# Optimization experiments

Hardware: AMD Instinct MI355X
Metric: run time of the kernel (lower is better)

Reference implementation:

```python
import jax, jax.numpy as jnp
import numpy as np

N = 50000
NEG_SLOPE = 0.2  # PyG GATConv default negative_slope


def _gat_layer(x, src, dst, edge_attr, W, We, a_src, a_dst, a_edge, bias):
    """Single-head PyG GATConv (heads=1, concat=True, add_self_loops=True,
    fill_value='mean' for self-loop edge_attr, dropout inactive / eval mode)."""
    n = x.shape[0]
    # add self loops; self-loop edge_attr = per-feature mean of edge_attr
    loop = jnp.arange(n)
    src2 = jnp.concatenate([src, loop])
    dst2 = jnp.concatenate([dst, loop])
    ea_loop = jnp.broadcast_to(edge_attr.mean(axis=0, keepdims=True), (n, edge_attr.shape[1]))
    ea = jnp.concatenate([edge_attr, ea_loop], axis=0)          # [E', edge_dim]

    h = x @ W                                                    # [N, C_out]
    a_s = h @ a_src                                              # [N]
    a_d = h @ a_dst                                              # [N]
    a_e = (ea @ We) @ a_edge                                     # [E']

    alpha = jax.nn.leaky_relu(a_s[src2] + a_d[dst2] + a_e, NEG_SLOPE)  # [E']
    # segment softmax over incoming edges of each dst node
    amax = jax.ops.segment_max(alpha, dst2, num_segments=n)     # [N]
    ex = jnp.exp(alpha - amax[dst2])                             # [E']
    denom = jax.ops.segment_sum(ex, dst2, num_segments=n)       # [N]
    w = ex / denom[dst2]                                         # [E']

    msg = h[src2] * w[:, None]                                   # [E', C_out]
    out = jax.ops.segment_sum(msg, dst2, num_segments=n) + bias  # [N, C_out]
    return out


def setup_inputs() -> dict:
    key = jax.random.key(0)
    ks = jax.random.split(key, 16)
    E, C_in, C_h, C_out, Ed = 800000, 128, 256, 128, 8
    s = 0.05
    inp = {
        "x": jax.random.normal(ks[0], (N, C_in), dtype=jnp.float32),
        "edge_index": jax.random.randint(ks[1], (2, E), 0, N, dtype=jnp.int32),
        "edge_attr": jax.random.normal(ks[2], (E, Ed), dtype=jnp.float32),
        # layer 1 params
        "W1": jax.random.normal(ks[3], (C_in, C_h), dtype=jnp.float32) * s,
        "We1": jax.random.normal(ks[4], (Ed, C_h), dtype=jnp.float32) * s,
        "as1": jax.random.normal(ks[5], (C_h,), dtype=jnp.float32) * s,
        "ad1": jax.random.normal(ks[6], (C_h,), dtype=jnp.float32) * s,
        "ae1": jax.random.normal(ks[7], (C_h,), dtype=jnp.float32) * s,
        "b1": jnp.zeros((C_h,), dtype=jnp.float32),
        # layer 2 params
        "W2": jax.random.normal(ks[8], (C_h, C_out), dtype=jnp.float32) * s,
        "We2": jax.random.normal(ks[9], (Ed, C_out), dtype=jnp.float32) * s,
        "as2": jax.random.normal(ks[10], (C_out,), dtype=jnp.float32) * s,
        "ad2": jax.random.normal(ks[11], (C_out,), dtype=jnp.float32) * s,
        "ae2": jax.random.normal(ks[12], (C_out,), dtype=jnp.float32) * s,
        "b2": jnp.zeros((C_out,), dtype=jnp.float32),
    }
    return inp


def reference(x, edge_index, edge_attr, W1, We1, as1, ad1, ae1, b1,
              W2, We2, as2, ad2, ae2, b2):
    src, dst = edge_index[0], edge_index[1]
    h = _gat_layer(x, src, dst, edge_attr, W1, We1, as1, ad1, ae1, b1)
    h = jax.nn.relu(h)  # relu between layers, not after last
    out = _gat_layer(h, src, dst, edge_attr, W2, We2, as2, ad2, ae2, b2)
    return out
```

## Files before the change

### kernel.cpp

```cpp
#include <hip/hip_runtime.h>
#include <hip/hip_bf16.h>


#define NEG_SLOPE 0.2f

typedef unsigned short u16;
typedef short short8 __attribute__((ext_vector_type(8)));
typedef float v4f __attribute__((ext_vector_type(4)));
typedef u16 u16x8 __attribute__((ext_vector_type(8)));

__device__ __forceinline__ u16 f2bf(float f) {
    unsigned u = __float_as_uint(f);
    return (u16)((u + 0x7fffu + ((u >> 16) & 1u)) >> 16);
}
__device__ __forceinline__ float bf2f(u16 h) {
    return __uint_as_float(((unsigned)h) << 16);
}
__device__ __forceinline__ float bf_lo(int v) { return __uint_as_float(((unsigned)v) << 16); }
__device__ __forceinline__ float bf_hi(int v) { return __uint_as_float(((unsigned)v) & 0xffff0000u); }
__device__ __forceinline__ float lrelu(float x) {
    return x >= 0.f ? x : NEG_SLOPE * x;
}
__device__ __forceinline__ int ld_acq(int* p) {
    return __hip_atomic_load(p, __ATOMIC_ACQUIRE, __HIP_MEMORY_SCOPE_AGENT);
}
__device__ __forceinline__ void st_rel(int* p, int v) {
    __hip_atomic_store(p, v, __ATOMIC_RELEASE, __HIP_MEMORY_SCOPE_AGENT);
}

__global__ __launch_bounds__(256) void prep_kernel(
        const float* __restrict__ W1, u16* __restrict__ w1thi, u16* __restrict__ w1tlo,
        const float* __restrict__ W2, u16* __restrict__ w2thi, u16* __restrict__ w2tlo,
        const float* __restrict__ We1, const float* __restrict__ ae1v,
        const float* __restrict__ We2, const float* __restrict__ ae2v,
        float* __restrict__ we_vec1g, float* __restrict__ we_vec2g) {
    int tid = threadIdx.x;
    if (blockIdx.x < 256) {
        int t = blockIdx.x * 256 + tid;
        if (t < 128 * 256) {
            int k = t >> 8, m = t & 255;
            float v = W1[t];
            u16 h = f2bf(v);
            w1thi[(size_t)m * 128 + k] = h;
            w1tlo[(size_t)m * 128 + k] = f2bf(v - bf2f(h));
        } else {
            t -= 128 * 256;
            int k = t >> 7, m = t & 127;
            float v = W2[t];
            u16 h = f2bf(v);
            w2thi[(size_t)m * 256 + k] = h;
            w2tlo[(size_t)m * 256 + k] = f2bf(v - bf2f(h));
        }
        return;
    }
    __shared__ float wv[16];
    if (tid < 16) wv[tid] = 0.f;
    __syncthreads();
    {
        float a1 = ae1v[tid];
        int lane = tid & 63;
#pragma unroll
        for (int j = 0; j < 8; ++j) {
            float v = We1[j * 256 + tid] * a1;
#pragma unroll
            for (int o = 32; o; o >>= 1) v += __shfl_down(v, o);
            if (lane == 0) atomicAdd(&wv[j], v);
        }
        if (tid < 128) {
            float a2 = ae2v[tid];
#pragma unroll
            for (int j = 0; j < 8; ++j) {
                float v = We2[j * 128 + tid] * a2;
#pragma unroll
                for (int o = 32; o; o >>= 1) v += __shfl_down(v, o);
                if (lane == 0) atomicAdd(&wv[8 + j], v);
            }
        }
    }
    __syncthreads();
    if (tid < 8)  we_vec1g[tid] = wv[tid];
    else if (tid < 16) we_vec2g[tid - 8] = wv[tid];
}

#define BK 32
#define LDA 40
__global__ __launch_bounds__(256) void fat1_kernel(
        const float* __restrict__ ea, const int* __restrict__ dst,
        float* __restrict__ mean_acc, int* __restrict__ deg,
        int* __restrict__ rank, float2* __restrict__ aEe, int E,
        const float* __restrict__ we_vec1g, const float* __restrict__ we_vec2g,
        int Fb, int Gg,
        const float* __restrict__ A32,
        const u16* __restrict__ Bh_g, const u16* __restrict__ Bl_g,
        u16* __restrict__ Cb, int Nrows, int K, int M,
        const float* __restrict__ av, const float* __restrict__ bv,
        float* __restrict__ as_out, float* __restrict__ ad_out, int gx) {
    __shared__ u16 Ah[64 * LDA];
    __shared__ u16 Bh[128 * LDA];
    __shared__ u16 Bl[128 * LDA];
    __shared__ float red[8];
    int tid = threadIdx.x;
    int bid = (int)blockIdx.x;
    int mn = Fb < Gg ? Fb : Gg;
    int hid = -1, gid = -1;
    if (bid < 2 * mn) {
        if ((bid & 1) == 0) hid = bid >> 1; else gid = bid >> 1;
    } else {
        int rem = bid - 2 * mn;
        if (Fb > Gg) hid = mn + rem; else gid = mn + rem;
    }
    if (hid >= 0) {
        float wv[16];
#pragma unroll
        for (int j = 0; j < 8; ++j) { wv[j] = we_vec1g[j]; wv[8 + j] = we_vec2g[j]; }
        if (tid < 8) red[tid] = 0.f;
        __syncthreads();
        float s[8] = {0.f};
        int stride = Fb * 256;
        for (int e = hid * 256 + tid; e < E; e += stride) {
            int d = dst[e];
            const float4 v0 = *(const float4*)&ea[(size_t)e * 8];
            const float4 v1 = *(const float4*)&ea[(size_t)e * 8 + 4];
            s[0] += v0.x; s[1] += v0.y; s[2] += v0.z; s[3] += v0.w;
            s[4] += v1.x; s[5] += v1.y; s[6] += v1.z; s[7] += v1.w;
            float s1 = v0.x * wv[0] + v0.y * wv[1] + v0.z * wv[2] + v0.w * wv[3]
                     + v1.x * wv[4] + v1.y * wv[5] + v1.z * wv[6] + v1.w * wv[7];
            float s2 = v0.x * wv[8] + v0.y * wv[9] + v0.z * wv[10] + v0.w * wv[11]
                     + v1.x * wv[12] + v1.y * wv[13] + v1.z * wv[14] + v1.w * wv[15];
            aEe[e] = make_float2(s1, s2);
            rank[e] = atomicAdd(&deg[d], 1);
        }
        int lane = tid & 63;
#pragma unroll
        for (int j = 0; j < 8; ++j) {
#pragma unroll
            for (int o = 32; o; o >>= 1) s[j] += __shfl_down(s[j], o);
            if (lane == 0) atomicAdd(&red[j], s[j]);
        }
        __syncthreads();
        if (tid < 8) atomicAdd(&mean_acc[tid], red[tid]);
        return;
    }
    int lane = tid & 63;
    int wvx = tid >> 6;
    int l15 = lane & 15, quad = lane >> 4;
    int rb = (gid / gx) * 64;
    int cb = (gid % gx) * 128;

    v4f acc[8];
#pragma unroll
    for (int ni = 0; ni < 8; ++ni) acc[ni] = (v4f){0.f, 0.f, 0.f, 0.f};

    int sr  = tid >> 2;
    int sc  = (tid & 3) * 8;
    int sr2 = tid >> 1;
    int sc2 = (tid & 1) * 16;

    for (int kc = 0; kc < K; kc += BK) {
        int gr = rb + sr;
        u16x8 a0 = {0,0,0,0,0,0,0,0};
        if (gr < Nrows) {
            const float* pa = A32 + (size_t)gr * K + kc + sc;
            float4 f0 = *(const float4*)pa;
            float4 f1 = *(const float4*)(pa + 4);
            a0 = (u16x8){f2bf(f0.x), f2bf(f0.y), f2bf(f0.z), f2bf(f0.w),
                         f2bf(f1.x), f2bf(f1.y), f2bf(f1.z), f2bf(f1.w)};
        }
        size_t bb = (size_t)(cb + sr2) * K + kc + sc2;
        u16x8 b0 = *(const u16x8*)(Bh_g + bb);
        u16x8 b1 = *(const u16x8*)(Bh_g + bb + 8);
        u16x8 b2 = *(const u16x8*)(Bl_g + bb);
        u16x8 b3 = *(const u16x8*)(Bl_g + bb + 8);
        *(u16x8*)&Ah[sr * LDA + sc] = a0;
        *(u16x8*)&Bh[sr2 * LDA + sc2] = b0;
        *(u16x8*)&Bh[sr2 * LDA + sc2 + 8] = b1;
        *(u16x8*)&Bl[sr2 * LDA + sc2] = b2;
        *(u16x8*)&Bl[sr2 * LDA + sc2 + 8] = b3;
        __syncthreads();
        short8 ah = *(const short8*)&Ah[(wvx * 16 + l15) * LDA + quad * 8];
#pragma unroll
        for (int ni = 0; ni < 8; ++ni) {
            int r = (ni * 16 + l15) * LDA + quad * 8;
            short8 bhf = *(const short8*)&Bh[r];
            short8 blf = *(const short8*)&Bl[r];
            acc[ni] = __builtin_amdgcn_mfma_f32_16x16x32_bf16(ah, bhf, acc[ni], 0, 0, 0);
            acc[ni] = __builtin_amdgcn_mfma_f32_16x16x32_bf16(ah, blf, acc[ni], 0, 0, 0);
        }
        __syncthreads();
    }
#pragma unroll
    for (int ni = 0; ni < 8; ++ni)
#pragma unroll
        for (int reg = 0; reg < 4; ++reg) {
            int row = rb + wvx * 16 + quad * 4 + reg;
            if (row < Nrows)
                Cb[(size_t)row * M + cb + ni * 16 + l15] = f2bf(acc[ni][reg]);
        }
    float sd[4] = {}, dd[4] = {};
#pragma unroll
    for (int ni = 0; ni < 8; ++ni) {
        int col = cb + ni * 16 + l15;
        float a = av[col], b = bv[col];
#pragma unroll
        for (int reg = 0; reg < 4; ++reg) {
            sd[reg] += acc[ni][reg] * a;
            dd[reg] += acc[ni][reg] * b;
        }
    }
#pragma unroll
    for (int off = 1; off < 16; off <<= 1)
#pragma unroll
        for (int reg = 0; reg < 4; ++reg) {
            sd[reg] += __shfl_xor(sd[reg], off);
            dd[reg] += __shfl_xor(dd[reg], off);
        }
    if (l15 == 0) {
        int row0 = rb + wvx * 16 + quad * 4;
#pragma unroll
        for (int reg = 0; reg < 4; ++reg)
            if (row0 + reg < Nrows) {
                atomicAdd(as_out + row0 + reg, sd[reg]);
                atomicAdd(ad_out + row0 + reg, dd[reg]);
            }
    }
}

__global__ __launch_bounds__(256) void scan_fused_kernel(
        const int* __restrict__ deg, int* __restrict__ row_start,
        int* __restrict__ partials, int* __restrict__ pprefix,
        int* __restrict__ gcount, int* __restrict__ gflag, int N, int n,
        const float* __restrict__ mean_acc, float Einv,
        const float* __restrict__ we_vec1, const float* __restrict__ we_vec2,
        float* __restrict__ ae_loop) {
    __shared__ int s[256];
    __shared__ int amLast, bprefix;
    int t = threadIdx.x, bid = blockIdx.x;
    int i = bid * 256 + t;
    int v = (i < N) ? deg[i] : 0;
    s[t] = v; __syncthreads();
    for (int off = 1; off < 256; off <<= 1) {
        int u = (t >= off) ? s[t - off] : 0;
        __syncthreads();
        s[t] += u;
        __syncthreads();
    }
    int incl = s[t];
    int total = s[255];
    if (t == 0) {
        partials[bid] = total;
        __threadfence();
        int c = __hip_atomic_fetch_add(gcount, 1, __ATOMIC_ACQ_REL, __HIP_MEMORY_SCOPE_AGENT);
        amLast = (c == (int)gridDim.x - 1);
    }
    __syncthreads();
    if (amLast) {
        int G = gridDim.x;
        int pv = (t < G) ? ld_acq(&partials[t]) : 0;
        __syncthreads();
        s[t] = pv; __syncthreads();
        for (int off = 1; off < 256; off <<= 1) {
            int u = (t >= off) ? s[t - off] : 0;
            __syncthreads();
            s[t] += u;
            __syncthreads();
        }
        if (t < G) pprefix[t] = s[t] - pv;
        if (t == 0) {
            float s1 = 0.f, s2 = 0.f;
#pragma unroll
            for (int j = 0; j < 8; ++j) {
                float m = mean_acc[j] * Einv;
                s1 += m * we_vec1[j];
                s2 += m * we_vec2[j];
            }
            ae_loop[0] = s1; ae_loop[1] = s2;
        }
        __threadfence();
        __syncthreads();
        if (t == 0) st_rel(gflag, 1);
    }
    if (t == 0) {
        while (ld_acq(gflag) == 0) __builtin_amdgcn_s_sleep(2);
        bprefix = ld_acq(&pprefix[bid]);
    }
    __syncthreads();
    int ex = bprefix + incl - v;
    if (i < n) row_start[i] = ex;
}

__global__ __launch_bounds__(256) void fill_kernel(
        const int* __restrict__ src, const int* __restrict__ dst,
        const float2* __restrict__ aEe, const int* __restrict__ row_start,
        const int* __restrict__ rank,
        const float* __restrict__ asv1, const float* __restrict__ adv1,
        float4* __restrict__ epack, int E) {
    int e = blockIdx.x * 256 + threadIdx.x;
    if (e >= E) return;
    int d = dst[e];
    int s = src[e];
    int idx = row_start[d] + rank[e];
    float2 a = aEe[e];
    float w = __expf(lrelu(asv1[s] + adv1[d] + a.x));
    epack[idx] = make_float4(__int_as_float(s), w, a.y, 0.f);
}

#define LDA2 40
__global__ __launch_bounds__(256) void gemm_mfma_kernel(
        const u16* __restrict__ A_g,
        const u16* __restrict__ Bh_g, const u16* __restrict__ Bl_g,
        u16* __restrict__ Cb, int Nrows, int K, int M,
        const float* __restrict__ av, const float* __restrict__ bv,
        float* __restrict__ as_out, float* __restrict__ ad_out) {
    __shared__ u16 Ah[128 * LDA2], Bh[128 * LDA2], Bl[128 * LDA2];
    int tid = threadIdx.x;
    int lane = tid & 63;
    int wv = tid >> 6;
    int wm = wv >> 1, wn = wv & 1;
    int l15 = lane & 15, quad = lane >> 4;
    int rb = blockIdx.y * 128;
    int cb = blockIdx.x * 128;

    v4f acc[4][4];
#pragma unroll
    for (int mi = 0; mi < 4; ++mi)
#pragma unroll
        for (int ni = 0; ni < 4; ++ni) acc[mi][ni] = (v4f){0.f, 0.f, 0.f, 0.f};

    int sr = tid >> 1;
    int sc = (tid & 1) * 16;

    for (int kc = 0; kc < K; kc += BK) {
        int gr = rb + sr;
        u16x8 a0 = {0,0,0,0,0,0,0,0}, a1 = {0,0,0,0,0,0,0,0};
        if (gr < Nrows) {
            size_t ba = (size_t)gr * K + kc + sc;
            a0 = *(const u16x8*)(A_g + ba);
            a1 = *(const u16x8*)(A_g + ba + 8);
        }
        size_t bb = (size_t)(cb + sr) * K + kc + sc;
        u16x8 b0 = *(const u16x8*)(Bh_g + bb);
        u16x8 b1 = *(const u16x8*)(Bh_g + bb + 8);
        u16x8 b2 = *(const u16x8*)(Bl_g + bb);
        u16x8 b3 = *(const u16x8*)(Bl_g + bb + 8);
        *(u16x8*)&Ah[sr * LDA2 + sc] = a0;
        *(u16x8*)&Ah[sr * LDA2 + sc + 8] = a1;
        *(u16x8*)&Bh[sr * LDA2 + sc] = b0;
        *(u16x8*)&Bh[sr * LDA2 + sc + 8] = b1;
        *(u16x8*)&Bl[sr * LDA2 + sc] = b2;
        *(u16x8*)&Bl[sr * LDA2 + sc + 8] = b3;
        __syncthreads();
        short8 ah[4], bh[4], bl[4];
#pragma unroll
        for (int mi = 0; mi < 4; ++mi)
            ah[mi] = *(const short8*)&Ah[(wm * 64 + mi * 16 + l15) * LDA2 + quad * 8];
#pragma unroll
        for (int ni = 0; ni < 4; ++ni) {
            int r = (wn * 64 + ni * 16 + l15) * LDA2 + quad * 8;
            bh[ni] = *(const short8*)&Bh[r];
            bl[ni] = *(const short8*)&Bl[r];
        }
#pragma unroll
        for (int mi = 0; mi < 4; ++mi)
#pragma unroll
            for (int ni = 0; ni < 4; ++ni) {
                acc[mi][ni] = __builtin_amdgcn_mfma_f32_16x16x32_bf16(ah[mi], bh[ni], acc[mi][ni], 0, 0, 0);
                acc[mi][ni] = __builtin_amdgcn_mfma_f32_16x16x32_bf16(ah[mi], bl[ni], acc[mi][ni], 0, 0, 0);
            }
        __syncthreads();
    }
#pragma unroll
    for (int mi = 0; mi < 4; ++mi)
#pragma unroll
        for (int ni = 0; ni < 4; ++ni)
#pragma unroll
            for (int reg = 0; reg < 4; ++reg) {
                int row = rb + wm * 64 + mi * 16 + quad * 4 + reg;
                if (row < Nrows)
                    Cb[(size_t)row * M + cb + wn * 64 + ni * 16 + l15] = f2bf(acc[mi][ni][reg]);
            }
    float sd[4][4] = {}, dd[4][4] = {};
#pragma unroll
    for (int ni = 0; ni < 4; ++ni) {
        int col = cb + wn * 64 + ni * 16 + l15;
        float a = av[col], b = bv[col];
#pragma unroll
        for (int mi = 0; mi < 4; ++mi)
#pragma unroll
            for (int reg = 0; reg < 4; ++reg) {
                sd[mi][reg] += acc[mi][ni][reg] * a;
                dd[mi][reg] += acc[mi][ni][reg] * b;
            }
    }
#pragma unroll
    for (int off = 1; off < 16; off <<= 1)
#pragma unroll
        for (int mi = 0; mi < 4; ++mi)
#pragma unroll
            for (int reg = 0; reg < 4; ++reg) {
                sd[mi][reg] += __shfl_xor(sd[mi][reg], off);
                dd[mi][reg] += __shfl_xor(dd[mi][reg], off);
            }
    if (l15 == 0)
#pragma unroll
        for (int mi = 0; mi < 4; ++mi) {
            int row0 = rb + wm * 64 + mi * 16 + quad * 4;
#pragma unroll
            for (int reg = 0; reg < 4; ++reg)
                if (row0 + reg < Nrows) {
                    atomicAdd(as_out + row0 + reg, sd[mi][reg]);
                    atomicAdd(ad_out + row0 + reg, dd[mi][reg]);
                }
        }
}

__global__ __launch_bounds__(256) void agg1_kernel(const int* __restrict__ row_start,
                                                   const float4* __restrict__ epack,
                                                   const float* __restrict__ asv,
                                                   const float* __restrict__ adv,
                                                   const float* __restrict__ ae_loop,
                                                   const u16* __restrict__ Hb,
                                                   u16* __restrict__ ohi,
                                                   const float* __restrict__ bias, int N) {
    __shared__ float2 xch[4][64];
    int lane = threadIdx.x & 63;
    int wvi = threadIdx.x >> 6;
    int node = blockIdx.x * 4 + wvi;
    if (node >= N) return;
    int st = row_start[node], en = row_start[node + 1];
    float wloop = __expf(lrelu(asv[node] + adv[node] + ae_loop[0]));
    float sum = wloop;
    int half = lane >> 5;
    int hl   = lane & 31;
    float acc[8];
    {
        int4 hv = *(const int4*)(Hb + (size_t)node * 256 + hl * 8);
        float w0 = half ? 0.f : wloop;
        acc[0] = w0 * bf_lo(hv.x); acc[1] = w0 * bf_hi(hv.x);
        acc[2] = w0 * bf_lo(hv.y); acc[3] = w0 * bf_hi(hv.y);
        acc[4] = w0 * bf_lo(hv.z); acc[5] = w0 * bf_hi(hv.z);
        acc[6] = w0 * bf_lo(hv.w); acc[7] = w0 * bf_hi(hv.w);
    }
    for (int base = st; base < en; base += 64) {
        int i = base + lane;
        float w = 0.f; int sreg = 0;
        if (i < en) {
            float4 ep = epack[i];
            sreg = __float_as_int(ep.x);
            w = ep.y;
        }
        float wsum = w;
#pragma unroll
        for (int o = 1; o < 64; o <<= 1) wsum += __shfl_xor(wsum, o);
        sum += wsum;
        xch[wvi][lane] = make_float2(w, __int_as_float(sreg));
        int cnt = min(64, en - base);
        int j = 0;
        for (; j + 8 <= cnt; j += 8) {
            float2 e[4]; int4 h[4];
#pragma unroll
            for (int q = 0; q < 4; ++q) e[q] = xch[wvi][j + 2 * q + half];
#pragma unroll
            for (int q = 0; q < 4; ++q)
                h[q] = *(const int4*)(Hb + (size_t)__float_as_int(e[q].y) * 256 + hl * 8);
#pragma unroll
            for (int q = 0; q < 4; ++q) {
                float w0 = e[q].x;
                acc[0] += w0 * bf_lo(h[q].x); acc[1] += w0 * bf_hi(h[q].x);
                acc[2] += w0 * bf_lo(h[q].y); acc[3] += w0 * bf_hi(h[q].y);
                acc[4] += w0 * bf_lo(h[q].z); acc[5] += w0 * bf_hi(h[q].z);
                acc[6] += w0 * bf_lo(h[q].w); acc[7] += w0 * bf_hi(h[q].w);
            }
        }
        for (; j + 2 <= cnt; j += 2) {
            float2 e0 = xch[wvi][j + half];
            int4 h0 = *(const int4*)(Hb + (size_t)__float_as_int(e0.y) * 256 + hl * 8);
            float w0 = e0.x;
            acc[0] += w0 * bf_lo(h0.x); acc[1] += w0 * bf_hi(h0.x);
            acc[2] += w0 * bf_lo(h0.y); acc[3] += w0 * bf_hi(h0.y);
            acc[4] += w0 * bf_lo(h0.z); acc[5] += w0 * bf_hi(h0.z);
            acc[6] += w0 * bf_lo(h0.w); acc[7] += w0 * bf_hi(h0.w);
        }
        if (j < cnt && half == 0) {
            float2 e0 = xch[wvi][j];
            int4 h0 = *(const int4*)(Hb + (size_t)__float_as_int(e0.y) * 256 + hl * 8);
            float w0 = e0.x;
            acc[0] += w0 * bf_lo(h0.x); acc[1] += w0 * bf_hi(h0.x);
            acc[2] += w0 * bf_lo(h0.y); acc[3] += w0 * bf_hi(h0.y);
            acc[4] += w0 * bf_lo(h0.z); acc[5] += w0 * bf_hi(h0.z);
            acc[6] += w0 * bf_lo(h0.w); acc[7] += w0 * bf_hi(h0.w);
        }
    }
#pragma unroll
    for (int c = 0; c < 8; ++c) acc[c] += __shfl_xor(acc[c], 32);
    if (half == 0) {
        float inv = 1.f / sum;
        const float4 b0 = *(const float4*)(bias + hl * 8);
        const float4 b1 = *(const float4*)(bias + hl * 8 + 4);
        float t0 = acc[0] * inv + b0.x, t1 = acc[1] * inv + b0.y;
        float t2 = acc[2] * inv + b0.z, t3 = acc[3] * inv + b0.w;
        float t4 = acc[4] * inv + b1.x, t5 = acc[5] * inv + b1.y;
        float t6 = acc[6] * inv + b1.z, t7 = acc[7] * inv + b1.w;
        t0 = t0 > 0.f ? t0 : 0.f; t1 = t1 > 0.f ? t1 : 0.f;
        t2 = t2 > 0.f ? t2 : 0.f; t3 = t3 > 0.f ? t3 : 0.f;
        t4 = t4 > 0.f ? t4 : 0.f; t5 = t5 > 0.f ? t5 : 0.f;
        t6 = t6 > 0.f ? t6 : 0.f; t7 = t7 > 0.f ? t7 : 0.f;
        u16x8 h;
        h[0] = f2bf(t0); h[1] = f2bf(t1); h[2] = f2bf(t2); h[3] = f2bf(t3);
        h[4] = f2bf(t4); h[5] = f2bf(t5); h[6] = f2bf(t6); h[7] = f2bf(t7);
        *(u16x8*)(ohi + (size_t)node * 256 + hl * 8) = h;
    }
}

__global__ __launch_bounds__(256) void agg2_kernel(const int* __restrict__ row_start,
                                                   const float4* __restrict__ epack,
                                                   const float* __restrict__ asv,
                                                   const float* __restrict__ adv,
                                                   const float* __restrict__ ae_loop,
                                                   const u16* __restrict__ Hb,
                                                   float* __restrict__ out,
                                                   const float* __restrict__ bias, int N) {
    __shared__ float2 xch[4][64];
    int lane = threadIdx.x & 63;
    int wvi = threadIdx.x >> 6;
    int node = blockIdx.x * 4 + wvi;
    if (node >= N) return;
    int st = row_start[node], en = row_start[node + 1];
    float ad = adv[node];
    float wloop = __expf(lrelu(asv[node] + ad + ae_loop[1]));
    float sum = wloop;
    int half = lane >> 5;
    int hl   = lane & 31;
    float acc[4];
    {
        int2 hv = *(const int2*)(Hb + (size_t)node * 128 + hl * 4);
        float w0 = half ? 0.f : wloop;
        acc[0] = w0 * bf_lo(hv.x); acc[1] = w0 * bf_hi(hv.x);
        acc[2] = w0 * bf_lo(hv.y); acc[3] = w0 * bf_hi(hv.y);
    }
    for (int base = st; base < en; base += 64) {
        int i = base + lane;
        float w = 0.f; int sreg = 0;
        if (i < en) {
            float4 ep = epack[i];
            sreg = __float_as_int(ep.x);
            w = __expf(lrelu(asv[sreg] + ad + ep.z));
        }
        float wsum = w;
#pragma unroll
        for (int o = 1; o < 64; o <<= 1) wsum += __shfl_xor(wsum, o);
        sum += wsum;
        xch[wvi][lane] = make_float2(w, __int_as_float(sreg));
        int cnt = min(64, en - base);
        int j = 0;
        for (; j + 8 <= cnt; j += 8) {
            float2 e[4]; int2 h[4];
#pragma unroll
            for (int q = 0; q < 4; ++q) e[q] = xch[wvi][j + 2 * q + half];
#pragma unroll
            for (int q = 0; q < 4; ++q)
                h[q] = *(const int2*)(Hb + (size_t)__float_as_int(e[q].y) * 128 + hl * 4);
#pragma unroll
            for (int q = 0; q < 4; ++q) {
                float w0 = e[q].x;
                acc[0] += w0 * bf_lo(h[q].x); acc[1] += w0 * bf_hi(h[q].x);
                acc[2] += w0 * bf_lo(h[q].y); acc[3] += w0 * bf_hi(h[q].y);
            }
        }
        for (; j + 2 <= cnt; j += 2) {
            float2 e0 = xch[wvi][j + half];
            int2 h0 = *(const int2*)(Hb + (size_t)__float_as_int(e0.y) * 128 + hl * 4);
            float w0 = e0.x;
            acc[0] += w0 * bf_lo(h0.x); acc[1] += w0 * bf_hi(h0.x);
            acc[2] += w0 * bf_lo(h0.y); acc[3] += w0 * bf_hi(h0.y);
        }
        if (j < cnt && half == 0) {
            float2 e0 = xch[wvi][j];
            int2 h0 = *(const int2*)(Hb + (size_t)__float_as_int(e0.y) * 128 + hl * 4);
            float w0 = e0.x;
            acc[0] += w0 * bf_lo(h0.x); acc[1] += w0 * bf_hi(h0.x);
            acc[2] += w0 * bf_lo(h0.y); acc[3] += w0 * bf_hi(h0.y);
        }
    }
#pragma unroll
    for (int c = 0; c < 4; ++c) acc[c] += __shfl_xor(acc[c], 32);
    if (half == 0) {
        float inv = 1.f / sum;
        const float4 bv = *(const float4*)(bias + hl * 4);
        float4 o;
        o.x = acc[0] * inv + bv.x;
        o.y = acc[1] * inv + bv.y;
        o.z = acc[2] * inv + bv.z;
        o.w = acc[3] * inv + bv.w;
        *(float4*)(out + (size_t)node * 128 + hl * 4) = o;
    }
}

extern "C" void kernel_launch(void* const* d_in, const int* in_sizes, int n_in,
                              void* d_out, int out_size, void* d_ws, size_t ws_size,
                              hipStream_t stream) {
    const int Cin = 128, Ch = 256, Co = 128;
    const int N = in_sizes[0] / Cin;
    const int E = in_sizes[1] / 2;

    const float* x   = (const float*)d_in[0];
    const int*   src = (const int*)d_in[1];
    const int*   dst = src + E;
    const float* ea  = (const float*)d_in[2];
    const float* W1  = (const float*)d_in[3];
    const float* We1 = (const float*)d_in[4];
    const float* as1 = (const float*)d_in[5];
    const float* ad1 = (const float*)d_in[6];
    const float* ae1 = (const float*)d_in[7];
    const float* b1  = (const float*)d_in[8];
    const float* W2  = (const float*)d_in[9];
    const float* We2 = (const float*)d_in[10];
    const float* as2 = (const float*)d_in[11];
    const float* ad2 = (const float*)d_in[12];
    const float* ae2 = (const float*)d_in[13];
    const float* b2  = (const float*)d_in[14];
    float* out = (float*)d_out;

    float* ws = (float*)d_ws;
    size_t off = 0;
    u16* h1b = (u16*)(ws + off); off += (size_t)N * Ch / 2;
    u16* g1b = (u16*)(ws + off); off += (size_t)N * Ch / 2;
    float4* epack = (float4*)(ws + off); off += (size_t)E * 4;
    float2* aEe   = (float2*)(ws + off); off += (size_t)E * 2;
    int* rank     = (int*)(ws + off); off += (size_t)E;
    int* row_start = (int*)(ws + off); off += (size_t)N + 1;
    int* partials  = (int*)(ws + off); off += 256;
    int* pprefix   = (int*)(ws + off); off += 256;
    u16* w1thi = (u16*)(ws + off); off += (size_t)Cin * Ch / 2;
    u16* w1tlo = (u16*)(ws + off); off += (size_t)Cin * Ch / 2;
    u16* w2thi = (u16*)(ws + off); off += (size_t)Ch * Co / 2;
    u16* w2tlo = (u16*)(ws + off); off += (size_t)Ch * Co / 2;
    int*   deg  = (int*)(ws + off); off += (size_t)N + 1;
    float* asv1 = ws + off; off += (size_t)N;
    float* adv1 = ws + off; off += (size_t)N;
    float* asv2 = ws + off; off += (size_t)N;
    float* adv2 = ws + off; off += (size_t)N;
    float* misc = ws + off; off += 32;
    float* mean_acc = misc;
    float* we_vec1  = misc + 8;
    float* we_vec2  = misc + 16;
    float* ae_loop  = misc + 24;
    int* gcount = (int*)(ws + off); off += 1;
    int* gflag  = (int*)(ws + off); off += 1;

    const int n1 = N + 1;
    const int nscan = (n1 + 255) / 256;

    hipMemsetAsync(deg, 0, ((size_t)5 * N + 35) * sizeof(float), stream);

    prep_kernel<<<257, 256, 0, stream>>>(
        W1, w1thi, w1tlo, W2, w2thi, w2tlo,
        We1, ae1, We2, ae2, we_vec1, we_vec2);

    {
        int Fb = 1024;
        int gx = Ch / 128;
        int Gg = gx * ((N + 63) / 64);
        fat1_kernel<<<Fb + Gg, 256, 0, stream>>>(
            ea, dst, mean_acc, deg, rank, aEe, E, we_vec1, we_vec2, Fb, Gg,
            x, w1thi, w1tlo, h1b, N, Cin, Ch, as1, ad1, asv1, adv1, gx);
    }

    scan_fused_kernel<<<nscan, 256, 0, stream>>>(
        deg, row_start, partials, pprefix, gcount, gflag, N, n1,
        mean_acc, 1.0f / (float)E, we_vec1, we_vec2, ae_loop);

    fill_kernel<<<(E + 255) / 256, 256, 0, stream>>>(src, dst, aEe, row_start,
                                                     rank, asv1, adv1, epack, E);

    agg1_kernel<<<(N + 3) / 4, 256, 0, stream>>>(row_start, epack, asv1, adv1, ae_loop,
                                                 h1b, g1b, b1, N);

    u16* h2b = h1b;
    {
        dim3 grid(Co / 128, (N + 127) / 128);
        gemm_mfma_kernel<<<grid, 256, 0, stream>>>(g1b, w2thi, w2tlo, h2b, N, Ch, Co,
                                                   as2, ad2, asv2, adv2);
    }
    agg2_kernel<<<(N + 3) / 4, 256, 0, stream>>>(row_start, epack, asv2, adv2, ae_loop,
                                                 h2b, out, b2, N);
}
```

Baseline: 343.6 us.

## Overlap layer-2 GEMM with agg1 tail and precompute layer-2 attention logits

Folds W2·as2 and W2·ad2 into 256-wide vectors so agg1 computes layer-2 source and destination scores directly from its bf16 output, dropping the atomic reductions in the GEMM epilogue. Splits agg1 at a node boundary and launches fused kernels that run the agg1 tail interleaved with GEMM tiles on finished rows, then the remaining GEMM tiles alongside a per-edge pass that precomputes layer-2 edge weights into epack. agg2 then reads the stored weight instead of recomputing the exp. This adds a separate h2b buffer and relies on kernel ordering for correctness, and the split point is hardcoded.

After: 369.9 us. 1.08x slower.

```diff
diff --git a/kernel.cpp b/kernel.cpp
--- a/kernel.cpp
+++ b/kernel.cpp
@@ -33,7 +33,9 @@
         const float* __restrict__ W2, u16* __restrict__ w2thi, u16* __restrict__ w2tlo,
         const float* __restrict__ We1, const float* __restrict__ ae1v,
         const float* __restrict__ We2, const float* __restrict__ ae2v,
-        float* __restrict__ we_vec1g, float* __restrict__ we_vec2g) {
+        float* __restrict__ we_vec1g, float* __restrict__ we_vec2g,
+        const float* __restrict__ as2v, const float* __restrict__ ad2v,
+        float* __restrict__ wa2g, float* __restrict__ wb2g) {
     int tid = threadIdx.x;
     if (blockIdx.x < 256) {
         int t = blockIdx.x * 256 + tid;
@@ -51,6 +53,20 @@
             w2thi[(size_t)m * 256 + k] = h;
             w2tlo[(size_t)m * 256 + k] = f2bf(v - bf2f(h));
         }
+        return;
+    }
+    if (blockIdx.x == 257) {
+        const float* w2row = W2 + (size_t)tid * 128;
+        float da = 0.f, db = 0.f;
+#pragma unroll 8
+        for (int m = 0; m < 128; m += 4) {
+            float4 w = *(const float4*)(w2row + m);
+            float4 a = *(const float4*)(as2v + m);
+            float4 b = *(const float4*)(ad2v + m);
+            da += w.x * a.x + w.y * a.y + w.z * a.z + w.w * a.w;
+            db += w.x * b.x + w.y * b.y + w.z * b.z + w.w * b.w;
+        }
+        wa2g[tid] = da; wb2g[tid] = db;
         return;
     }
     __shared__ float wv[16];
@@ -304,128 +320,15 @@
     epack[idx] = make_float4(__int_as_float(s), w, a.y, 0.f);
 }
 
-#define LDA2 40
-__global__ __launch_bounds__(256) void gemm_mfma_kernel(
-        const u16* __restrict__ A_g,
-        const u16* __restrict__ Bh_g, const u16* __restrict__ Bl_g,
-        u16* __restrict__ Cb, int Nrows, int K, int M,
-        const float* __restrict__ av, const float* __restrict__ bv,
-        float* __restrict__ as_out, float* __restrict__ ad_out) {
-    __shared__ u16 Ah[128 * LDA2], Bh[128 * LDA2], Bl[128 * LDA2];
-    int tid = threadIdx.x;
-    int lane = tid & 63;
-    int wv = tid >> 6;
-    int wm = wv >> 1, wn = wv & 1;
-    int l15 = lane & 15, quad = lane >> 4;
-    int rb = blockIdx.y * 128;
-    int cb = blockIdx.x * 128;
-
-    v4f acc[4][4];
-#pragma unroll
-    for (int mi = 0; mi < 4; ++mi)
-#pragma unroll
-        for (int ni = 0; ni < 4; ++ni) acc[mi][ni] = (v4f){0.f, 0.f, 0.f, 0.f};
-
-    int sr = tid >> 1;
-    int sc = (tid & 1) * 16;
-
-    for (int kc = 0; kc < K; kc += BK) {
-        int gr = rb + sr;
-        u16x8 a0 = {0,0,0,0,0,0,0,0}, a1 = {0,0,0,0,0,0,0,0};
-        if (gr < Nrows) {
-            size_t ba = (size_t)gr * K + kc + sc;
-            a0 = *(const u16x8*)(A_g + ba);
-            a1 = *(const u16x8*)(A_g + ba + 8);
-        }
-        size_t bb = (size_t)(cb + sr) * K + kc + sc;
-        u16x8 b0 = *(const u16x8*)(Bh_g + bb);
-        u16x8 b1 = *(const u16x8*)(Bh_g + bb + 8);
-        u16x8 b2 = *(const u16x8*)(Bl_g + bb);
-        u16x8 b3 = *(const u16x8*)(Bl_g + bb + 8);
-        *(u16x8*)&Ah[sr * LDA2 + sc] = a0;
-        *(u16x8*)&Ah[sr * LDA2 + sc + 8] = a1;
-        *(u16x8*)&Bh[sr * LDA2 + sc] = b0;
-        *(u16x8*)&Bh[sr * LDA2 + sc + 8] = b1;
-        *(u16x8*)&Bl[sr * LDA2 + sc] = b2;
-        *(u16x8*)&Bl[sr * LDA2 + sc + 8] = b3;
-        __syncthreads();
-        short8 ah[4], bh[4], bl[4];
-#pragma unroll
-        for (int mi = 0; mi < 4; ++mi)
-            ah[mi] = *(const short8*)&Ah[(wm * 64 + mi * 16 + l15) * LDA2 + quad * 8];
-#pragma unroll
-        for (int ni = 0; ni < 4; ++ni) {
-            int r = (wn * 64 + ni * 16 + l15) * LDA2 + quad * 8;
-            bh[ni] = *(const short8*)&Bh[r];
-            bl[ni] = *(const short8*)&Bl[r];
-        }
-#pragma unroll
-        for (int mi = 0; mi < 4; ++mi)
-#pragma unroll
-            for (int ni = 0; ni < 4; ++ni) {
-                acc[mi][ni] = __builtin_amdgcn_mfma_f32_16x16x32_bf16(ah[mi], bh[ni], acc[mi][ni], 0, 0, 0);
-                acc[mi][ni] = __builtin_amdgcn_mfma_f32_16x16x32_bf16(ah[mi], bl[ni], acc[mi][ni], 0, 0, 0);
-            }
-        __syncthreads();
-    }
-#pragma unroll
-    for (int mi = 0; mi < 4; ++mi)
-#pragma unroll
-        for (int ni = 0; ni < 4; ++ni)
-#pragma unroll
-            for (int reg = 0; reg < 4; ++reg) {
-                int row = rb + wm * 64 + mi * 16 + quad * 4 + reg;
-                if (row < Nrows)
-                    Cb[(size_t)row * M + cb + wn * 64 + ni * 16 + l15] = f2bf(acc[mi][ni][reg]);
-            }
-    float sd[4][4] = {}, dd[4][4] = {};
-#pragma unroll
-    for (int ni = 0; ni < 4; ++ni) {
-        int col = cb + wn * 64 + ni * 16 + l15;
-        float a = av[col], b = bv[col];
-#pragma unroll
-        for (int mi = 0; mi < 4; ++mi)
-#pragma unroll
-            for (int reg = 0; reg < 4; ++reg) {
-                sd[mi][reg] += acc[mi][ni][reg] * a;
-                dd[mi][reg] += acc[mi][ni][reg] * b;
-            }
-    }
-#pragma unroll
-    for (int off = 1; off < 16; off <<= 1)
-#pragma unroll
-        for (int mi = 0; mi < 4; ++mi)
-#pragma unroll
-            for (int reg = 0; reg < 4; ++reg) {
-                sd[mi][reg] += __shfl_xor(sd[mi][reg], off);
-                dd[mi][reg] += __shfl_xor(dd[mi][reg], off);
-            }
-    if (l15 == 0)
-#pragma unroll
-        for (int mi = 0; mi < 4; ++mi) {
-            int row0 = rb + wm * 64 + mi * 16 + quad * 4;
-#pragma unroll
-            for (int reg = 0; reg < 4; ++reg)
-                if (row0 + reg < Nrows) {
-                    atomicAdd(as_out + row0 + reg, sd[mi][reg]);
-                    atomicAdd(ad_out + row0 + reg, dd[mi][reg]);
-                }
-        }
-}
-
-__global__ __launch_bounds__(256) void agg1_kernel(const int* __restrict__ row_start,
-                                                   const float4* __restrict__ epack,
-                                                   const float* __restrict__ asv,
-                                                   const float* __restrict__ adv,
-                                                   const float* __restrict__ ae_loop,
-                                                   const u16* __restrict__ Hb,
-                                                   u16* __restrict__ ohi,
-                                                   const float* __restrict__ bias, int N) {
-    __shared__ float2 xch[4][64];
-    int lane = threadIdx.x & 63;
-    int wvi = threadIdx.x >> 6;
-    int node = blockIdx.x * 4 + wvi;
-    if (node >= N) return;
+__device__ __forceinline__ void agg1_node(
+        int node, int lane, float2* xw,
+        const int* __restrict__ row_start, const float4* __restrict__ epack,
+        const float* __restrict__ asv, const float* __restrict__ adv,
+        const float* __restrict__ ae_loop,
+        const u16* __restrict__ Hb, u16* __restrict__ ohi,
+        const float* __restrict__ bias,
+        const float* __restrict__ wa2, const float* __restrict__ wb2,
+        float* __restrict__ asv2, float* __restrict__ adv2) {
     int st = row_start[node], en = row_start[node + 1];
     float wloop = __expf(lrelu(asv[node] + adv[node] + ae_loop[0]));
     float sum = wloop;
@@ -452,27 +355,27 @@
 #pragma unroll
         for (int o = 1; o < 64; o <<= 1) wsum += __shfl_xor(wsum, o);
         sum += wsum;
-        xch[wvi][lane] = make_float2(w, __int_as_float(sreg));
-        int cnt = min(64, en - base);
+        xw[lane] = make_float2(w, __int_as_float(sreg));
+        int cnt = en - base; if (cnt > 64) cnt = 64;
         int j = 0;
         for (; j + 8 <= cnt; j += 8) {
-            float2 e[4]; int4 h[4];
-#pragma unroll
-            for (int q = 0; q < 4; ++q) e[q] = xch[wvi][j + 2 * q + half];
+            float2 e[4]; int4 h4[4];
+#pragma unroll
+            for (int q = 0; q < 4; ++q) e[q] = xw[j + 2 * q + half];
 #pragma unroll
             for (int q = 0; q < 4; ++q)
-                h[q] = *(const int4*)(Hb + (size_t)__float_as_int(e[q].y) * 256 + hl * 8);
+                h4[q] = *(const int4*)(Hb + (size_t)__float_as_int(e[q].y) * 256 + hl * 8);
 #pragma unroll
             for (int q = 0; q < 4; ++q) {
                 float w0 = e[q].x;
-                acc[0] += w0 * bf_lo(h[q].x); acc[1] += w0 * bf_hi(h[q].x);
-                acc[2] += w0 * bf_lo(h[q].y); acc[3] += w0 * bf_hi(h[q].y);
-                acc[4] += w0 * bf_lo(h[q].z); acc[5] += w0 * bf_hi(h[q].z);
-                acc[6] += w0 * bf_lo(h[q].w); acc[7] += w0 * bf_hi(h[q].w);
+                acc[0] += w0 * bf_lo(h4[q].x); acc[1] += w0 * bf_hi(h4[q].x);
+                acc[2] += w0 * bf_lo(h4[q].y); acc[3] += w0 * bf_hi(h4[q].y);
+                acc[4] += w0 * bf_lo(h4[q].z); acc[5] += w0 * bf_hi(h4[q].z);
+                acc[6] += w0 * bf_lo(h4[q].w); acc[7] += w0 * bf_hi(h4[q].w);
             }
         }
         for (; j + 2 <= cnt; j += 2) {
-            float2 e0 = xch[wvi][j + half];
+            float2 e0 = xw[j + half];
             int4 h0 = *(const int4*)(Hb + (size_t)__float_as_int(e0.y) * 256 + hl * 8);
             float w0 = e0.x;
             acc[0] += w0 * bf_lo(h0.x); acc[1] += w0 * bf_hi(h0.x);
@@ -481,7 +384,7 @@
             acc[6] += w0 * bf_lo(h0.w); acc[7] += w0 * bf_hi(h0.w);
         }
         if (j < cnt && half == 0) {
-            float2 e0 = xch[wvi][j];
+            float2 e0 = xw[j];
             int4 h0 = *(const int4*)(Hb + (size_t)__float_as_int(e0.y) * 256 + hl * 8);
             float w0 = e0.x;
             acc[0] += w0 * bf_lo(h0.x); acc[1] += w0 * bf_hi(h0.x);
@@ -504,11 +407,152 @@
         t2 = t2 > 0.f ? t2 : 0.f; t3 = t3 > 0.f ? t3 : 0.f;
         t4 = t4 > 0.f ? t4 : 0.f; t5 = t5 > 0.f ? t5 : 0.f;
         t6 = t6 > 0.f ? t6 : 0.f; t7 = t7 > 0.f ? t7 : 0.f;
-        u16x8 h;
-        h[0] = f2bf(t0); h[1] = f2bf(t1); h[2] = f2bf(t2); h[3] = f2bf(t3);
-        h[4] = f2bf(t4); h[5] = f2bf(t5); h[6] = f2bf(t6); h[7] = f2bf(t7);
-        *(u16x8*)(ohi + (size_t)node * 256 + hl * 8) = h;
-    }
+        u16x8 hv8;
+        hv8[0] = f2bf(t0); hv8[1] = f2bf(t1); hv8[2] = f2bf(t2); hv8[3] = f2bf(t3);
+        hv8[4] = f2bf(t4); hv8[5] = f2bf(t5); hv8[6] = f2bf(t6); hv8[7] = f2bf(t7);
+        *(u16x8*)(ohi + (size_t)node * 256 + hl * 8) = hv8;
+        const float* wa = wa2 + hl * 8;
+        const float* wb = wb2 + hl * 8;
+        float da = 0.f, db = 0.f;
+#pragma unroll
+        for (int c = 0; c < 8; ++c) {
+            float r = bf2f(hv8[c]);
+            da += r * wa[c]; db += r * wb[c];
+        }
+#pragma unroll
+        for (int o = 1; o < 32; o <<= 1) {
+            da += __shfl_xor(da, o);
+            db += __shfl_xor(db, o);
+        }
+        if (hl == 0) { asv2[node] = da; adv2[node] = db; }
+    }
+}
+
+__global__ __launch_bounds__(256) void agg1_kernel(
+        int n0, int ncap,
+        const int* __restrict__ row_start, const float4* __restrict__ epack,
+        const float* __restrict__ asv, const float* __restrict__ adv,
+        const float* __restrict__ ae_loop,
+        const u16* __restrict__ Hb, u16* __restrict__ ohi,
+        const float* __restrict__ bias,
+        const float* __restrict__ wa2, const float* __restrict__ wb2,
+        float* __restrict__ asv2, float* __restrict__ adv2) {
+    __shared__ float2 xch[4][64];
+    int lane = threadIdx.x & 63;
+    int wvi = threadIdx.x >> 6;
+    int node = n0 + blockIdx.x * 4 + wvi;
+    if (node >= ncap) return;
+    agg1_node(node, lane, xch[wvi], row_start, epack, asv, adv, ae_loop,
+              Hb, ohi, bias, wa2, wb2, asv2, adv2);
+}
+
+__device__ __forceinline__ void gemm2_tile(
+        int gid, int r0, int Nrows, int tid,
+        const u16* __restrict__ A_g, const u16* __restrict__ Bh_g,
+        const u16* __restrict__ Bl_g, u16* __restrict__ Cb,
+        u16* Ah, u16* Bh, u16* Bl) {
+    const int K = 256, M = 128;
+    int lane = tid & 63;
+    int wvx = tid >> 6;
+    int l15 = lane & 15, quad = lane >> 4;
+    int rb = r0 + gid * 64;
+    v4f acc[8];
+#pragma unroll
+    for (int ni = 0; ni < 8; ++ni) acc[ni] = (v4f){0.f, 0.f, 0.f, 0.f};
+    int sr  = tid >> 2;
+    int sc  = (tid & 3) * 8;
+    int sr2 = tid >> 1;
+    int sc2 = (tid & 1) * 16;
+    for (int kc = 0; kc < K; kc += BK) {
+        int gr = rb + sr;
+        u16x8 a0 = {0,0,0,0,0,0,0,0};
+        if (gr < Nrows) a0 = *(const u16x8*)(A_g + (size_t)gr * K + kc + sc);
+        size_t bb = (size_t)sr2 * K + kc + sc2;
+        u16x8 b0 = *(const u16x8*)(Bh_g + bb);
+        u16x8 b1 = *(const u16x8*)(Bh_g + bb + 8);
+        u16x8 b2 = *(const u16x8*)(Bl_g + bb);
+        u16x8 b3 = *(const u16x8*)(Bl_g + bb + 8);
+        *(u16x8*)&Ah[sr * LDA + sc] = a0;
+        *(u16x8*)&Bh[sr2 * LDA + sc2] = b0;
+        *(u16x8*)&Bh[sr2 * LDA + sc2 + 8] = b1;
+        *(u16x8*)&Bl[sr2 * LDA + sc2] = b2;
+        *(u16x8*)&Bl[sr2 * LDA + sc2 + 8] = b3;
+        __syncthreads();
+        short8 ah = *(const short8*)&Ah[(wvx * 16 + l15) * LDA + quad * 8];
+#pragma unroll
+        for (int ni = 0; ni < 8; ++ni) {
+            int r = (ni * 16 + l15) * LDA + quad * 8;
+            short8 bhf = *(const short8*)&Bh[r];
+            short8 blf = *(const short8*)&Bl[r];
+            acc[ni] = __builtin_amdgcn_mfma_f32_16x16x32_bf16(ah, bhf, acc[ni], 0, 0, 0);
+            acc[ni] = __builtin_amdgcn_mfma_f32_16x16x32_bf16(ah, blf, acc[ni], 0, 0, 0);
+        }
+        __syncthreads();
+    }
+#pragma unroll
+    for (int ni = 0; ni < 8; ++ni)
+#pragma unroll
+        for (int reg = 0; reg < 4; ++reg) {
+            int row = rb + wvx * 16 + quad * 4 + reg;
+            if (row < Nrows)
+                Cb[(size_t)row * M + ni * 16 + l15] = f2bf(acc[ni][reg]);
+        }
+}
+
+__global__ __launch_bounds__(256) void fat23_kernel(
+        int Ga, int n0a, int Ncap,
+        int Gg, int r0g, int NrowsG,
+        int Ge,
+        const int* __restrict__ row_start, const float4* __restrict__ epack,
+        const float* __restrict__ asv1v, const float* __restrict__ adv1v,
+        const float* __restrict__ ae_loop,
+        const u16* __restrict__ h1b, u16* __restrict__ g1b,
+        const float* __restrict__ b1,
+        const float* __restrict__ wa2, const float* __restrict__ wb2,
+        float* __restrict__ asv2, float* __restrict__ adv2,
+        const u16* __restrict__ Ag, const u16* __restrict__ Bh_g,
+        const u16* __restrict__ Bl_g, u16* __restrict__ Cb,
+        const int* __restrict__ src, const int* __restrict__ dst,
+        const int* __restrict__ rank, const float2* __restrict__ aEe,
+        float4* __restrict__ epackw, int E) {
+    __shared__ u16 Ah[64 * LDA];
+    __shared__ u16 Bh[128 * LDA];
+    __shared__ u16 Bl[128 * LDA];
+    int tid = threadIdx.x;
+    int bid = (int)blockIdx.x;
+    int aid = -1, gid = -1, eid = -1;
+    if (bid < Ga + Gg) {
+        int mn = Ga < Gg ? Ga : Gg;
+        if (bid < 2 * mn) {
+            if (bid & 1) gid = bid >> 1; else aid = bid >> 1;
+        } else {
+            int rem = bid - 2 * mn;
+            if (Ga > Gg) aid = mn + rem; else gid = mn + rem;
+        }
+    } else {
+        eid = bid - (Ga + Gg);
+    }
+    if (aid >= 0) {
+        float2 (*xch)[64] = (float2(*)[64])Ah;
+        int lane = tid & 63;
+        int wvi = tid >> 6;
+        int node = n0a + aid * 4 + wvi;
+        if (node >= Ncap) return;
+        agg1_node(node, lane, xch[wvi], row_start, epack, asv1v, adv1v, ae_loop,
+                  h1b, g1b, b1, wa2, wb2, asv2, adv2);
+        return;
+    }
+    if (eid >= 0) {
+        int e = eid * 256 + tid;
+        if (e < E) {
+            int d = dst[e], s = src[e];
+            int i = row_start[d] + rank[e];
+            float w = __expf(lrelu(asv2[s] + adv2[d] + aEe[e].y));
+            ((float*)(epackw + i))[2] = w;
+        }
+        return;
+    }
+    gemm2_tile(gid, r0g, NrowsG, tid, Ag, Bh_g, Bl_g, Cb, Ah, Bh, Bl);
 }
 
 __global__ __launch_bounds__(256) void agg2_kernel(const int* __restrict__ row_start,
@@ -525,8 +569,7 @@
     int node = blockIdx.x * 4 + wvi;
     if (node >= N) return;
     int st = row_start[node], en = row_start[node + 1];
-    float ad = adv[node];
-    float wloop = __expf(lrelu(asv[node] + ad + ae_loop[1]));
+    float wloop = __expf(lrelu(asv[node] + adv[node] + ae_loop[1]));
     float sum = wloop;
     int half = lane >> 5;
     int hl   = lane & 31;
@@ -543,14 +586,14 @@
         if (i < en) {
             float4 ep = epack[i];
             sreg = __float_as_int(ep.x);
-            w = __expf(lrelu(asv[sreg] + ad + ep.z));
+            w = ep.z;
         }
         float wsum = w;
 #pragma unroll
         for (int o = 1; o < 64; o <<= 1) wsum += __shfl_xor(wsum, o);
         sum += wsum;
         xch[wvi][lane] = make_float2(w, __int_as_float(sreg));
-        int cnt = min(64, en - base);
+        int cnt = en - base; if (cnt > 64) cnt = 64;
         int j = 0;
         for (; j + 8 <= cnt; j += 8) {
             float2 e[4]; int2 h[4];
@@ -624,12 +667,15 @@
     size_t off = 0;
     u16* h1b = (u16*)(ws + off); off += (size_t)N * Ch / 2;
     u16* g1b = (u16*)(ws + off); off += (size_t)N * Ch / 2;
+    u16* h2b = (u16*)(ws + off); off += (size_t)N * Co / 2;
     float4* epack = (float4*)(ws + off); off += (size_t)E * 4;
     float2* aEe   = (float2*)(ws + off); off += (size_t)E * 2;
     int* rank     = (int*)(ws + off); off += (size_t)E;
     int* row_start = (int*)(ws + off); off += (size_t)N + 1;
     int* partials  = (int*)(ws + off); off += 256;
     int* pprefix   = (int*)(ws + off); off += 256;
+    float* wa2 = ws + off; off += 256;
+    float* wb2 = ws + off; off += 256;
     u16* w1thi = (u16*)(ws + off); off += (size_t)Cin * Ch / 2;
     u16* w1tlo = (u16*)(ws + off); off += (size_t)Cin * Ch / 2;
     u16* w2thi = (u16*)(ws + off); off += (size_t)Ch * Co / 2;
@@ -652,9 +698,9 @@
 
     hipMemsetAsync(deg, 0, ((size_t)5 * N + 35) * sizeof(float), stream);
 
-    prep_kernel<<<257, 256, 0, stream>>>(
+    prep_kernel<<<258, 256, 0, stream>>>(
         W1, w1thi, w1tlo, W2, w2thi, w2tlo,
-        We1, ae1, We2, ae2, we_vec1, we_vec2);
+        We1, ae1, We2, ae2, we_vec1, we_vec2, as2, ad2, wa2, wb2);
 
     {
         int Fb = 1024;
@@ -672,15 +718,32 @@
     fill_kernel<<<(E + 255) / 256, 256, 0, stream>>>(src, dst, aEe, row_start,
                                                      rank, asv1, adv1, epack, E);
 
-    agg1_kernel<<<(N + 3) / 4, 256, 0, stream>>>(row_start, epack, asv1, adv1, ae_loop,
-                                                 h1b, g1b, b1, N);
-
-    u16* h2b = h1b;
+    const int Nh = 35072;
+    agg1_kernel<<<Nh / 4, 256, 0, stream>>>(
+        0, Nh, row_start, epack, asv1, adv1, ae_loop,
+        h1b, g1b, b1, wa2, wb2, asv2, adv2);
+
     {
-        dim3 grid(Co / 128, (N + 127) / 128);
-        gemm_mfma_kernel<<<grid, 256, 0, stream>>>(g1b, w2thi, w2tlo, h2b, N, Ch, Co,
-                                                   as2, ad2, asv2, adv2);
-    }
+        int Ga = (N - Nh + 3) / 4;
+        int Gg0 = Nh / 64;
+        fat23_kernel<<<Ga + Gg0, 256, 0, stream>>>(
+            Ga, Nh, N, Gg0, 0, Nh, 0,
+            row_start, epack, asv1, adv1, ae_loop, h1b, g1b, b1,
+            wa2, wb2, asv2, adv2,
+            g1b, w2thi, w2tlo, h2b,
+            src, dst, rank, aEe, epack, E);
+    }
+    {
+        int Gg1 = (N - Nh + 63) / 64;
+        int Ge = (E + 255) / 256;
+        fat23_kernel<<<Gg1 + Ge, 256, 0, stream>>>(
+            0, 0, N, Gg1, Nh, N, Ge,
+            row_start, epack, asv1, adv1, ae_loop, h1b, g1b, b1,
+            wa2, wb2, asv2, adv2,
+            g1b, w2thi, w2tlo, h2b,
+            src, dst, rank, aEe, epack, E);
+    }
+
     agg2_kernel<<<(N + 3) / 4, 256, 0, stream>>>(row_start, epack, asv2, adv2, ae_loop,
                                                  h2b, out, b2, N);
 }
```
